# Optimization experiments

Hardware: AMD Instinct MI355X
Metric: run time of the kernel (lower is better)

The kernel has to match this reference:

```python
import jax, jax.numpy as jnp
import numpy as np

B, H, O, E, CMAP = 8192, 1024, 256, 16, 1000


def setup_inputs() -> dict:
    key = jax.random.key(0)
    k_x, k_w, k_b, k_num, k_c = jax.random.split(key, 5)
    x = jax.random.normal(k_x, (B, H), dtype=jnp.float32)
    num = jax.random.randint(k_num, (B,), 0, CMAP, dtype=jnp.int64)
    c = jax.random.randint(k_c, (CMAP,), 0, E, dtype=jnp.int64)
    # per-expert Linear params (torch default: uniform(-1/sqrt(H), 1/sqrt(H)))
    bound = 1.0 / np.sqrt(H)
    W = jax.random.uniform(k_w, (E, O, H), dtype=jnp.float32, minval=-bound, maxval=bound)
    b = jax.random.uniform(k_b, (E, O), dtype=jnp.float32, minval=-bound, maxval=bound)
    return {"x": x, "W": W, "b": b, "num": num, "c": c}


def reference(x, W, b, num, c):
    # expert id for each sample: layers[c[num[i]]]
    expert = c[num]  # [B]
    # compute all experts' linear outputs in one batched GEMM, then select.
    # logits: [B, E, O]
    logits = jnp.einsum('bh,eoh->beo', x, W) + b[None, :, :]
    sel = jnp.take_along_axis(logits, expert[:, None, None], axis=1)[:, 0, :]  # [B, O]
    return jax.nn.sigmoid(sel)
```

## Files before the change

### kernel.cpp

```cpp
#include <hip/hip_runtime.h>
#include <hip/hip_bf16.h>
#include <stdint.h>

#define B_N   8192
#define H_K   1024
#define O_N   256
#define E_N   16
#define RCAP  1024

#define TILE_M    32
#define TILE_N    128
#define BK        64
#define NITER     (H_K / BK)
#define MTILES    (RCAP / TILE_M)

#define WS_CURSOR   0
#define WS_ROWBUF   1024
#define WS_WBF16    131072

typedef __attribute__((ext_vector_type(8))) short  short8;
typedef __attribute__((ext_vector_type(4))) float  float4v;

__device__ __forceinline__ short f32_to_bf16(float f) {
    uint32_t u = __builtin_bit_cast(uint32_t, f);
    u += 0x7fffu + ((u >> 16) & 1u);
    return (short)(u >> 16);
}

__device__ __forceinline__ short8 cvt8(float4v v0, float4v v1) {
    short8 s;
    s[0] = f32_to_bf16(v0[0]); s[1] = f32_to_bf16(v0[1]);
    s[2] = f32_to_bf16(v0[2]); s[3] = f32_to_bf16(v0[3]);
    s[4] = f32_to_bf16(v1[0]); s[5] = f32_to_bf16(v1[1]);
    s[6] = f32_to_bf16(v1[2]); s[7] = f32_to_bf16(v1[3]);
    return s;
}

__device__ __forceinline__ float4v mfma16(short8 a, short8 b, float4v c) {
    return __builtin_amdgcn_mfma_f32_16x16x32_bf16(a, b, c, 0, 0, 0);
}

__device__ __forceinline__ void gl2lds16(const void* gsrc, void* ldst) {
    __builtin_amdgcn_global_load_lds(
        (const __attribute__((address_space(1))) uint32_t*)gsrc,
        (__attribute__((address_space(3))) uint32_t*)ldst, 16, 0, 0);
}

__global__ __launch_bounds__(256) void
k_prep(const float* __restrict__ W, const int* __restrict__ num, const int* __restrict__ c,
       int* __restrict__ cursor, int* __restrict__ rowbuf, short* __restrict__ Wb) {
    const int tid = threadIdx.x;
    const int bx  = blockIdx.x;

    if (bx < E_N) {
        unsigned mask = 0;
#pragma unroll
        for (int u = 0; u < 32; ++u) {
            const int i = u * 256 + tid;
            const int e = c[num[i]];
            mask |= (unsigned)(e == bx) << u;
        }
        const int cnt = __popc(mask);
        const int lane = tid & 63, wv = tid >> 6;
        int incl = cnt;
#pragma unroll
        for (int d = 1; d < 64; d <<= 1) {
            int v = __shfl_up(incl, d, 64);
            if (lane >= d) incl += v;
        }
        __shared__ int wsum[4];
        if (lane == 63) wsum[wv] = incl;
        __syncthreads();
        int base = 0;
        for (int w = 0; w < wv; ++w) base += wsum[w];
        int pos = base + incl - cnt;
        for (int u = 0; u < 32; ++u)
            if ((mask >> u) & 1u) rowbuf[bx * RCAP + pos++] = u * 256 + tid;
        if (tid == 255) cursor[bx] = base + incl;
    }

    const int nchunk = E_N * O_N * H_K / 8;
    const int stride = 256 * 256;
    for (int ch = bx * 256 + tid; ch < nchunk; ch += stride) {
        const float4v* src = (const float4v*)(W + (size_t)ch * 8);
        *(short8*)(Wb + (size_t)ch * 8) = cvt8(src[0], src[1]);
    }
}

__global__ __launch_bounds__(256, 4) void
k_gemm(const float* __restrict__ x, const short* __restrict__ Wb,
       const float* __restrict__ bias, const int* __restrict__ cursor,
       const int* __restrict__ rowbuf, float* __restrict__ out) {
    const int e = blockIdx.x;
    int count = cursor[e]; if (count > RCAP) count = RCAP;
    const int m0 = blockIdx.y * TILE_M;
    if (m0 >= count) return;
    const int n0 = blockIdx.z * TILE_N;

    __shared__ short xs[2][TILE_M][BK];
    __shared__ short wsh[2][TILE_N][BK];

    const int tid = threadIdx.x;
    const int r8  = tid >> 3;
    const int c8  = tid & 7;
    const int xrow = (m0 + r8 < count) ? rowbuf[e * RCAP + m0 + r8] : -1;
    const int xphys = (c8 ^ (r8 & 7)) * 8;

    const int lane = tid & 63;
    const int wave = tid >> 6;
    const int wm = wave >> 1, wn = wave & 1;
    const int quad = lane >> 4, l16 = lane & 15;

    const int sub = lane >> 3;
    const int clx = (lane & 7) ^ sub;

    const short* wseg = Wb + (size_t)(e * O_N + n0) * H_K;

    float4v xv0, xv1;
    auto load_x = [&](int k0) {
        if (xrow >= 0) {
            const float4v* p = (const float4v*)(x + (size_t)xrow * H_K + k0 + c8 * 8);
            xv0 = p[0]; xv1 = p[1];
        } else { xv0 = (float4v)0.0f; xv1 = (float4v)0.0f; }
    };
    auto store_x = [&](int buf) {
        *(short8*)&xs[buf][r8][xphys] = cvt8(xv0, xv1);
    };
    auto issue_w = [&](int buf, int k0) {
#pragma unroll
        for (int u = 0; u < 4; ++u) {
            const int q = wave * 4 + u;
            gl2lds16(wseg + (size_t)(q * 8 + sub) * H_K + k0 + clx * 8,
                     &wsh[buf][q * 8][0]);
        }
    };

    float4v acc[4];
#pragma unroll
    for (int j = 0; j < 4; ++j) acc[j] = (float4v)0.0f;

    load_x(0);
    issue_w(0, 0);
    store_x(0);

    for (int k = 0; k < NITER; ++k) {
        const int cur = k & 1;
        __syncthreads();
        if (k + 1 < NITER) {
            load_x((k + 1) * BK);
            issue_w(1 - cur, (k + 1) * BK);
        }

#pragma unroll
        for (int ks = 0; ks < 2; ++ks) {
            const int cl = ks * 4 + quad;
            const int cx = (cl ^ (l16 & 7)) * 8;
            short8 a  = *(const short8*)&xs[cur][wm * 16 + l16][cx];
            short8 b0 = *(const short8*)&wsh[cur][wn * 64 + l16][cx];
            short8 b1 = *(const short8*)&wsh[cur][wn * 64 + 16 + l16][cx];
            short8 b2 = *(const short8*)&wsh[cur][wn * 64 + 32 + l16][cx];
            short8 b3 = *(const short8*)&wsh[cur][wn * 64 + 48 + l16][cx];
            acc[0] = mfma16(a, b0, acc[0]);
            acc[1] = mfma16(a, b1, acc[1]);
            acc[2] = mfma16(a, b2, acc[2]);
            acc[3] = mfma16(a, b3, acc[3]);
        }

        if (k + 1 < NITER) store_x(1 - cur);
    }

#pragma unroll
    for (int j = 0; j < 4; ++j) {
        const int colg = n0 + wn * 64 + j * 16 + l16;
        const float bv = bias[e * O_N + colg];
#pragma unroll
        for (int reg = 0; reg < 4; ++reg) {
            const int pos = m0 + wm * 16 + quad * 4 + reg;
            if (pos < count) {
                const int rid = rowbuf[e * RCAP + pos];
                const float v = acc[j][reg] + bv;
                out[(size_t)rid * O_N + colg] = 1.0f / (1.0f + __expf(-v));
            }
        }
    }
}

extern "C" void kernel_launch(void* const* d_in, const int* in_sizes, int n_in,
                              void* d_out, int out_size, void* d_ws, size_t ws_size,
                              hipStream_t stream) {
    const float* x   = (const float*)d_in[0];
    const float* W   = (const float*)d_in[1];
    const float* b   = (const float*)d_in[2];
    const int*   num = (const int*)d_in[3];
    const int*   c   = (const int*)d_in[4];
    float* out = (float*)d_out;

    char*  ws     = (char*)d_ws;
    int*   cursor = (int*)(ws + WS_CURSOR);
    int*   rowbuf = (int*)(ws + WS_ROWBUF);
    short* Wb     = (short*)(ws + WS_WBF16);

    k_prep<<<256, 256, 0, stream>>>(W, num, c, cursor, rowbuf, Wb);

    dim3 gg(E_N, MTILES, O_N / TILE_N);
    k_gemm<<<gg, 256, 0, stream>>>(x, Wb, b, cursor, rowbuf, out);
}
```

Measured before the change: 118.2 us.

## Fuse fp32-to-bf16 weight conversion into GEMM tile loads, drop prep pass

Removes the separate pass that converted all expert weights to bf16 in workspace. The GEMM now loads fp32 weights straight into registers, converts them and stores them swizzled into LDS, double-buffered like the activations. This saves a full read and write of the weight tensor plus a kernel's worth of conversion work. In exchange each GEMM block re-reads fp32 weights (twice the bytes) and converts them redundantly across M-tiles, uses more registers (occupancy hint lowered from 4 to 3), and loses the async global-to-LDS path.

```diff
diff --git a/kernel.cpp b/kernel.cpp
--- a/kernel.cpp
+++ b/kernel.cpp
@@ -1,5 +1,4 @@
 #include <hip/hip_runtime.h>
-#include <hip/hip_bf16.h>
 #include <stdint.h>
 
 #define B_N   8192
@@ -16,7 +15,6 @@
 
 #define WS_CURSOR   0
 #define WS_ROWBUF   1024
-#define WS_WBF16    131072
 
 typedef __attribute__((ext_vector_type(8))) short  short8;
 typedef __attribute__((ext_vector_type(4))) float  float4v;
@@ -40,55 +38,40 @@
     return __builtin_amdgcn_mfma_f32_16x16x32_bf16(a, b, c, 0, 0, 0);
 }
 
-__device__ __forceinline__ void gl2lds16(const void* gsrc, void* ldst) {
-    __builtin_amdgcn_global_load_lds(
-        (const __attribute__((address_space(1))) uint32_t*)gsrc,
-        (__attribute__((address_space(3))) uint32_t*)ldst, 16, 0, 0);
-}
-
 __global__ __launch_bounds__(256) void
-k_prep(const float* __restrict__ W, const int* __restrict__ num, const int* __restrict__ c,
-       int* __restrict__ cursor, int* __restrict__ rowbuf, short* __restrict__ Wb) {
+k_bucket(const int* __restrict__ num, const int* __restrict__ c,
+         int* __restrict__ cursor, int* __restrict__ rowbuf) {
     const int tid = threadIdx.x;
     const int bx  = blockIdx.x;
 
-    if (bx < E_N) {
-        unsigned mask = 0;
-#pragma unroll
-        for (int u = 0; u < 32; ++u) {
-            const int i = u * 256 + tid;
-            const int e = c[num[i]];
-            mask |= (unsigned)(e == bx) << u;
-        }
-        const int cnt = __popc(mask);
-        const int lane = tid & 63, wv = tid >> 6;
-        int incl = cnt;
-#pragma unroll
-        for (int d = 1; d < 64; d <<= 1) {
-            int v = __shfl_up(incl, d, 64);
-            if (lane >= d) incl += v;
-        }
-        __shared__ int wsum[4];
-        if (lane == 63) wsum[wv] = incl;
-        __syncthreads();
-        int base = 0;
-        for (int w = 0; w < wv; ++w) base += wsum[w];
-        int pos = base + incl - cnt;
-        for (int u = 0; u < 32; ++u)
-            if ((mask >> u) & 1u) rowbuf[bx * RCAP + pos++] = u * 256 + tid;
-        if (tid == 255) cursor[bx] = base + incl;
-    }
-
-    const int nchunk = E_N * O_N * H_K / 8;
-    const int stride = 256 * 256;
-    for (int ch = bx * 256 + tid; ch < nchunk; ch += stride) {
-        const float4v* src = (const float4v*)(W + (size_t)ch * 8);
-        *(short8*)(Wb + (size_t)ch * 8) = cvt8(src[0], src[1]);
-    }
-}
-
-__global__ __launch_bounds__(256, 4) void
-k_gemm(const float* __restrict__ x, const short* __restrict__ Wb,
+    unsigned mask = 0;
+#pragma unroll
+    for (int u = 0; u < 32; ++u) {
+        const int i = u * 256 + tid;
+        const int e = c[num[i]];
+        mask |= (unsigned)(e == bx) << u;
+    }
+    const int cnt = __popc(mask);
+    const int lane = tid & 63, wv = tid >> 6;
+    int incl = cnt;
+#pragma unroll
+    for (int d = 1; d < 64; d <<= 1) {
+        int v = __shfl_up(incl, d, 64);
+        if (lane >= d) incl += v;
+    }
+    __shared__ int wsum[4];
+    if (lane == 63) wsum[wv] = incl;
+    __syncthreads();
+    int base = 0;
+    for (int w = 0; w < wv; ++w) base += wsum[w];
+    int pos = base + incl - cnt;
+    for (int u = 0; u < 32; ++u)
+        if ((mask >> u) & 1u) rowbuf[bx * RCAP + pos++] = u * 256 + tid;
+    if (tid == 255) cursor[bx] = base + incl;
+}
+
+__global__ __launch_bounds__(256, 3) void
+k_gemm(const float* __restrict__ x, const float* __restrict__ W,
        const float* __restrict__ bias, const int* __restrict__ cursor,
        const int* __restrict__ rowbuf, float* __restrict__ out) {
     const int e = blockIdx.x;
@@ -101,6 +84,7 @@
     __shared__ short wsh[2][TILE_N][BK];
 
     const int tid = threadIdx.x;
+
     const int r8  = tid >> 3;
     const int c8  = tid & 7;
     const int xrow = (m0 + r8 < count) ? rowbuf[e * RCAP + m0 + r8] : -1;
@@ -111,12 +95,13 @@
     const int wm = wave >> 1, wn = wave & 1;
     const int quad = lane >> 4, l16 = lane & 15;
 
-    const int sub = lane >> 3;
-    const int clx = (lane & 7) ^ sub;
-
-    const short* wseg = Wb + (size_t)(e * O_N + n0) * H_K;
+    const int wr = tid >> 2;
+    const int wq = tid & 3;
+    const float* wseg = W + (size_t)(e * O_N + n0) * H_K;
 
     float4v xv0, xv1;
+    float4v wv[2][4];
+
     auto load_x = [&](int k0) {
         if (xrow >= 0) {
             const float4v* p = (const float4v*)(x + (size_t)xrow * H_K + k0 + c8 * 8);
@@ -126,12 +111,22 @@
     auto store_x = [&](int buf) {
         *(short8*)&xs[buf][r8][xphys] = cvt8(xv0, xv1);
     };
-    auto issue_w = [&](int buf, int k0) {
-#pragma unroll
-        for (int u = 0; u < 4; ++u) {
-            const int q = wave * 4 + u;
-            gl2lds16(wseg + (size_t)(q * 8 + sub) * H_K + k0 + clx * 8,
-                     &wsh[buf][q * 8][0]);
+    auto load_w = [&](int k0) {
+#pragma unroll
+        for (int p = 0; p < 2; ++p) {
+            const float* src = wseg + (size_t)(p * 64 + wr) * H_K + k0 + wq * 16;
+#pragma unroll
+            for (int j = 0; j < 4; ++j) wv[p][j] = *(const float4v*)(src + j * 4);
+        }
+    };
+    auto store_w = [&](int buf) {
+#pragma unroll
+        for (int p = 0; p < 2; ++p) {
+            const int row = p * 64 + wr;
+            const int ph0 = ((wq * 2)     ^ (row & 7)) * 8;
+            const int ph1 = ((wq * 2 + 1) ^ (row & 7)) * 8;
+            *(short8*)&wsh[buf][row][ph0] = cvt8(wv[p][0], wv[p][1]);
+            *(short8*)&wsh[buf][row][ph1] = cvt8(wv[p][2], wv[p][3]);
         }
     };
 
@@ -140,15 +135,16 @@
     for (int j = 0; j < 4; ++j) acc[j] = (float4v)0.0f;
 
     load_x(0);
-    issue_w(0, 0);
+    load_w(0);
     store_x(0);
+    store_w(0);
 
     for (int k = 0; k < NITER; ++k) {
         const int cur = k & 1;
         __syncthreads();
         if (k + 1 < NITER) {
             load_x((k + 1) * BK);
-            issue_w(1 - cur, (k + 1) * BK);
+            load_w((k + 1) * BK);
         }
 
 #pragma unroll
@@ -166,7 +162,10 @@
             acc[3] = mfma16(a, b3, acc[3]);
         }
 
-        if (k + 1 < NITER) store_x(1 - cur);
+        if (k + 1 < NITER) {
+            store_x(1 - cur);
+            store_w(1 - cur);
+        }
     }
 
 #pragma unroll
@@ -198,10 +197,9 @@
     char*  ws     = (char*)d_ws;
     int*   cursor = (int*)(ws + WS_CURSOR);
     int*   rowbuf = (int*)(ws + WS_ROWBUF);
-    short* Wb     = (short*)(ws + WS_WBF16);
-
-    k_prep<<<256, 256, 0, stream>>>(W, num, c, cursor, rowbuf, Wb);
+
+    k_bucket<<<16, 256, 0, stream>>>(num, c, cursor, rowbuf);
 
     dim3 gg(E_N, MTILES, O_N / TILE_N);
-    k_gemm<<<gg, 256, 0, stream>>>(x, Wb, b, cursor, rowbuf, out);
-}
+    k_gemm<<<gg, 256, 0, stream>>>(x, W, b, cursor, rowbuf, out);
+}
```

Result: slower. 128.4 us (+8.7%).
